# Optimization experiments

Hardware: AMD Instinct MI355X
Metric: run time of the kernel (lower is better)

The kernel has to match this reference:

```python
import jax, jax.numpy as jnp
import numpy as np

ALPHA = 0.2  # LeakyReLU negative slope


def setup_inputs() -> dict:
    key = jax.random.key(0)
    k1, k2, k3, k4 = jax.random.split(key, 4)
    B, N, F_IN, F_OUT = 4, 4096, 256, 256
    h = jax.random.normal(k1, (B, N, F_IN), dtype=jnp.float32)
    adj = jax.random.randint(k2, (B, N, N), 0, 2, dtype=jnp.int32)
    # xavier_normal with gain=1.414: std = gain*sqrt(2/(fan_in+fan_out))
    std_W = 1.414 * np.sqrt(2.0 / (F_IN + F_OUT))
    W = jax.random.normal(k3, (F_IN, F_OUT), dtype=jnp.float32) * std_W
    std_a = 1.414 * np.sqrt(2.0 / (1 + 2 * F_OUT))
    a = jax.random.normal(k4, (1, 2 * F_OUT), dtype=jnp.float32) * std_a
    return {"h": h, "adj": adj, "W": W, "a": a}


def reference(h, adj, W, a):
    # h: [B, N, F_in], adj: [B, N, N] (0/1), W: [F_in, F_out], a: [1, 2*F_out]
    F_out = W.shape[1]
    Hh = jnp.einsum('bni,io->bno', h, W)               # [B, N, F_out]
    a_src = a[0, :F_out]                                # attends to edge source i
    a_dst = a[0, F_out:]                                # attends to edge target j
    s = jnp.einsum('bno,o->bn', Hh, a_src)              # [B, N]
    d = jnp.einsum('bno,o->bn', Hh, a_dst)              # [B, N]
    # score(i,j) = a . concat(Hh_i, Hh_j) = s_i + d_j
    logits = s[:, :, None] + d[:, None, :]              # [B, N, N]
    # edge_e = exp(-leakyrelu(score)) only on edges (adj nonzero), else 0
    e = jnp.where(adj != 0,
                  jnp.exp(-jax.nn.leaky_relu(logits, negative_slope=ALPHA)),
                  jnp.zeros((), dtype=Hh.dtype))        # [B, N, N]
    rowsum = jnp.sum(e, axis=-1, keepdims=True)         # [B, N, 1]
    # rows with zero sum keep divisor 1 (as in the torch code)
    rowsum = jnp.where(rowsum == 0.0, 1.0, rowsum)
    h_prime = jnp.einsum('bnm,bmo->bno', e, Hh) / rowsum  # [B, N, F_out]
    return jax.nn.elu(h_prime)  # concat=True branch
```

## Files before the change

kernel.cpp:

```cpp
#include <hip/hip_runtime.h>

#define LRELU_ALPHA 0.2f

typedef __bf16 bf16x8 __attribute__((ext_vector_type(8)));
typedef unsigned short u16;
typedef unsigned short u16x4 __attribute__((ext_vector_type(4)));
typedef unsigned short u16x8 __attribute__((ext_vector_type(8)));
typedef unsigned int   u32x2 __attribute__((ext_vector_type(2)));
typedef float f32x4 __attribute__((ext_vector_type(4)));
typedef int int4v __attribute__((ext_vector_type(4)));

__device__ __forceinline__ u16 f2bf(float f) {
  unsigned int u = __float_as_uint(f);
  u += 0x7fffu + ((u >> 16) & 1u);
  return (u16)(u >> 16);
}

__global__ __launch_bounds__(256) void wcast(const float* __restrict__ W,
                                             u16* __restrict__ WbT) {
  int idx = blockIdx.x * 256 + threadIdx.x;
  WbT[idx] = f2bf(W[(idx & 255) * 256 + (idx >> 8)]);
}

__global__ __launch_bounds__(256) void gemm1(const float* __restrict__ h,
                                             const u16* __restrict__ WbT,
                                             const float* __restrict__ a,
                                             u16* __restrict__ HhT,
                                             float* __restrict__ sbuf,
                                             float* __restrict__ dbuf) {
  const int tid = threadIdx.x, bid = blockIdx.x;
  const int l = tid & 63, w = tid >> 6;
  const int lr = l & 15;
  const int lk = (l >> 4) << 3;
  const int rowA = bid * 64 + 16 * w + lr;
  const float* hrow = h + (size_t)rowA * 256 + lk;

  f32x4 acc[16];
#pragma unroll
  for (int n = 0; n < 16; ++n) acc[n] = (f32x4){0.f, 0.f, 0.f, 0.f};

  for (int k0 = 0; k0 < 256; k0 += 32) {
    f32x4 a0 = *(const f32x4*)(hrow + k0);
    f32x4 a1 = *(const f32x4*)(hrow + k0 + 4);
    u16x8 au;
    au[0] = f2bf(a0[0]); au[1] = f2bf(a0[1]); au[2] = f2bf(a0[2]); au[3] = f2bf(a0[3]);
    au[4] = f2bf(a1[0]); au[5] = f2bf(a1[1]); au[6] = f2bf(a1[2]); au[7] = f2bf(a1[3]);
    bf16x8 af = __builtin_bit_cast(bf16x8, au);
#pragma unroll
    for (int n = 0; n < 16; ++n) {
      int4v bv = *(const int4v*)(WbT + (size_t)(16 * n + lr) * 256 + k0 + lk);
      bf16x8 bf = __builtin_bit_cast(bf16x8, bv);
      acc[n] = __builtin_amdgcn_mfma_f32_16x16x32_bf16(af, bf, acc[n], 0, 0, 0);
    }
  }

  float sp[4] = {0.f, 0.f, 0.f, 0.f}, dp[4] = {0.f, 0.f, 0.f, 0.f};
#pragma unroll
  for (int n = 0; n < 16; ++n) {
    int col = 16 * n + lr;
    float as = a[col];
    float ad = a[256 + col];
#pragma unroll
    for (int rr = 0; rr < 4; ++rr) {
      int row = bid * 64 + 16 * w + ((l >> 4) << 2) + rr;
      int bb = row >> 12, nl = row & 4095;
      float v = acc[n][rr];
      HhT[((size_t)(bb * 256 + col)) * 4096 + nl] = f2bf(v);
      sp[rr] += v * as;
      dp[rr] += v * ad;
    }
  }
#pragma unroll
  for (int rr = 0; rr < 4; ++rr) {
#pragma unroll
    for (int off = 1; off < 16; off <<= 1) {
      sp[rr] += __shfl_xor(sp[rr], off);
      dp[rr] += __shfl_xor(dp[rr], off);
    }
  }
  if ((l & 15) == 0) {
#pragma unroll
    for (int rr = 0; rr < 4; ++rr) {
      int row = bid * 64 + 16 * w + ((l >> 4) << 2) + rr;
      sbuf[row] = sp[rr];
      dbuf[row] = dp[rr];
    }
  }
}

__global__ __launch_bounds__(256, 2) void gat_main(const int* __restrict__ adj,
                                                   const u16* __restrict__ HhT,
                                                   const float* __restrict__ s,
                                                   const float* __restrict__ d,
                                                   float* __restrict__ out) {
  __shared__ __align__(16) u16 At[2][32 * 40];
  __shared__ __align__(16) u16 Bt[2][256 * 40];
  __shared__ float d_lds[4096];
  __shared__ float rs_lds[32];

  const int tid = threadIdx.x;
  const int bid = blockIdx.x;
  const int xcd = bid & 7;
  const int b = xcd >> 1;
  const int tile = (bid >> 3) | ((xcd & 1) << 6);
  const int rowbase = tile << 5;

  for (int i = tid; i < 4096; i += 256) d_lds[i] = d[b * 4096 + i];

  const int r = tid >> 3, q = tid & 7;
  const float s_row = s[b * 4096 + rowbase + r];

  const int4v* aptr = (const int4v*)(adj + ((size_t)(b * 4096 + rowbase + r)) * 4096);
  const int cr = tid >> 2, cp = tid & 3;
  const int4v* bp0 = (const int4v*)HhT + (((size_t)(b * 256 + cr      )) << 9) + cp;
  const int4v* bp1 = (const int4v*)HhT + (((size_t)(b * 256 + cr +  64)) << 9) + cp;
  const int4v* bp2 = (const int4v*)HhT + (((size_t)(b * 256 + cr + 128)) << 9) + cp;
  const int4v* bp3 = (const int4v*)HhT + (((size_t)(b * 256 + cr + 192)) << 9) + cp;

  const int l = tid & 63, w = tid >> 6;
  const int lr = l & 15, lk = (l >> 4) << 3;
  const int row0 = 16 * (w & 1);
  const int colb = 128 * (w >> 1);

  f32x4 acc[8];
#pragma unroll
  for (int n = 0; n < 8; ++n) acc[n] = (f32x4){0.f, 0.f, 0.f, 0.f};
  float rowacc = 0.f;

  __syncthreads();

  int4v pa_a = aptr[q],        pa_b = aptr[8 + q];
  int4v pb0_a = bp0[0], pb1_a = bp1[0], pb2_a = bp2[0], pb3_a = bp3[0];
  int4v pb0_b = bp0[4], pb1_b = bp1[4], pb2_b = bp2[4], pb3_b = bp3[4];

#define SUBSTEP(BUF, PA, PB0, PB1, PB2, PB3, CURSTEP, NEXTSTEP)               \
  {                                                                           \
    const int k0_ = (CURSTEP) << 5;                                           \
    f32x4 dv = *(const f32x4*)&d_lds[k0_ + q * 4];                            \
    int aj[4] = {PA.x, PA.y, PA.z, PA.w};                                     \
    u16x4 ep;                                                                 \
    _Pragma("unroll")                                                         \
    for (int j = 0; j < 4; ++j) {                                             \
      float lg = s_row + dv[j];                                               \
      float t = lg > 0.f ? lg : LRELU_ALPHA * lg;                             \
      float e = (aj[j] != 0) ? __expf(-t) : 0.f;                              \
      rowacc += e;                                                            \
      ep[j] = f2bf(e);                                                        \
    }                                                                         \
    *(u32x2*)&At[BUF][r * 40 + q * 4] = __builtin_bit_cast(u32x2, ep);        \
    *(int4v*)&Bt[BUF][(cr      ) * 40 + cp * 8] = PB0;                        \
    *(int4v*)&Bt[BUF][(cr +  64) * 40 + cp * 8] = PB1;                        \
    *(int4v*)&Bt[BUF][(cr + 128) * 40 + cp * 8] = PB2;                        \
    *(int4v*)&Bt[BUF][(cr + 192) * 40 + cp * 8] = PB3;                        \
    {                                                                         \
      const int ns_ = (NEXTSTEP);                                             \
      PA  = aptr[ns_ * 8 + q];                                                \
      PB0 = bp0[ns_ << 2];                                                    \
      PB1 = bp1[ns_ << 2];                                                    \
      PB2 = bp2[ns_ << 2];                                                    \
      PB3 = bp3[ns_ << 2];                                                    \
    }                                                                         \
    asm volatile("s_waitcnt lgkmcnt(0)" ::: "memory");                        \
    __builtin_amdgcn_s_barrier();                                             \
    {                                                                         \
      bf16x8 af = __builtin_bit_cast(bf16x8,                                  \
          *(const int4v*)&At[BUF][(row0 + lr) * 40 + lk]);                    \
      _Pragma("unroll")                                                       \
      for (int n = 0; n < 8; ++n) {                                           \
        bf16x8 bf = __builtin_bit_cast(bf16x8,                                \
            *(const int4v*)&Bt[BUF][(colb + 16 * n + lr) * 40 + lk]);         \
        acc[n] = __builtin_amdgcn_mfma_f32_16x16x32_bf16(af, bf, acc[n],      \
                                                         0, 0, 0);            \
      }                                                                       \
    }                                                                         \
  }

  for (int sp2 = 0; sp2 < 128; sp2 += 2) {
    int na = sp2 + 2; if (na > 127) na = 127;
    int nb = sp2 + 3; if (nb > 127) nb = 127;
    SUBSTEP(0, pa_a, pb0_a, pb1_a, pb2_a, pb3_a, sp2, na)
    SUBSTEP(1, pa_b, pb0_b, pb1_b, pb2_b, pb3_b, sp2 + 1, nb)
  }
#undef SUBSTEP

  float rsum = rowacc;
  rsum += __shfl_xor(rsum, 1);
  rsum += __shfl_xor(rsum, 2);
  rsum += __shfl_xor(rsum, 4);
  if (q == 0) rs_lds[r] = (rsum == 0.f) ? 1.f : rsum;
  __syncthreads();

#pragma unroll
  for (int rr = 0; rr < 4; ++rr) {
    int rin = row0 + ((l >> 4) << 2) + rr;
    float inv = 1.f / rs_lds[rin];
    size_t obase = ((size_t)(b * 4096 + rowbase + rin)) * 256 + colb;
#pragma unroll
    for (int n = 0; n < 8; ++n) {
      float v = acc[n][rr] * inv;
      out[obase + 16 * n + lr] = v > 0.f ? v : (__expf(v) - 1.f);
    }
  }
}

extern "C" void kernel_launch(void* const* d_in, const int* in_sizes, int n_in,
                              void* d_out, int out_size, void* d_ws, size_t ws_size,
                              hipStream_t stream) {
  const float* h = (const float*)d_in[0];
  const int* adj = (const int*)d_in[1];
  const float* W = (const float*)d_in[2];
  const float* a = (const float*)d_in[3];
  float* out = (float*)d_out;

  u16* WbT  = (u16*)d_ws;
  u16* HhT  = (u16*)((char*)d_ws + 131072);
  float* sb = (float*)((char*)d_ws + 131072 + 8388608);
  float* db = sb + 16384;

  hipLaunchKernelGGL(wcast,    dim3(256), dim3(256), 0, stream, W, WbT);
  hipLaunchKernelGGL(gemm1,    dim3(256), dim3(256), 0, stream, h, WbT, a, HhT, sb, db);
  hipLaunchKernelGGL(gat_main, dim3(512), dim3(256), 0, stream, adj, HhT, sb, db, out);
}
```

Measured before the change: 176.9 us.

## Compute attention weights directly in MFMA A-fragment registers and deepen prefetch

Each lane now computes the exp(-leakyrelu) edge weights for exactly the A-fragment elements it feeds to the MFMA, so the A tile no longer round-trips through LDS and the d vector is read from global memory instead of staged in shared memory. Adjacency, d and HhT loads are prefetched four steps ahead instead of two, and setprio plus sched_barrier are added around the MFMA block. The cost is that each weight is computed redundantly by the two wave columns (waves 0/2 and 1/3 share rows), and register pressure grows with more prefetch buffers, which could hurt occupancy at the 256x2 launch bound.

```diff
diff --git a/kernel.cpp b/kernel.cpp
--- a/kernel.cpp
+++ b/kernel.cpp
@@ -4,9 +4,7 @@
 
 typedef __bf16 bf16x8 __attribute__((ext_vector_type(8)));
 typedef unsigned short u16;
-typedef unsigned short u16x4 __attribute__((ext_vector_type(4)));
 typedef unsigned short u16x8 __attribute__((ext_vector_type(8)));
-typedef unsigned int   u32x2 __attribute__((ext_vector_type(2)));
 typedef float f32x4 __attribute__((ext_vector_type(4)));
 typedef int int4v __attribute__((ext_vector_type(4)));
 
@@ -93,9 +91,7 @@
                                                    const float* __restrict__ s,
                                                    const float* __restrict__ d,
                                                    float* __restrict__ out) {
-  __shared__ __align__(16) u16 At[2][32 * 40];
   __shared__ __align__(16) u16 Bt[2][256 * 40];
-  __shared__ float d_lds[4096];
   __shared__ float rs_lds[32];
 
   const int tid = threadIdx.x;
@@ -105,66 +101,73 @@
   const int tile = (bid >> 3) | ((xcd & 1) << 6);
   const int rowbase = tile << 5;
 
-  for (int i = tid; i < 4096; i += 256) d_lds[i] = d[b * 4096 + i];
-
-  const int r = tid >> 3, q = tid & 7;
-  const float s_row = s[b * 4096 + rowbase + r];
-
-  const int4v* aptr = (const int4v*)(adj + ((size_t)(b * 4096 + rowbase + r)) * 4096);
+  const int l = tid & 63, w = tid >> 6;
+  const int lr = l & 15, lkg = l >> 4, lk = lkg << 3;
+  const int row0 = 16 * (w & 1);
+  const int colb = 128 * (w >> 1);
+
+  const int myrow = rowbase + row0 + lr;
+  const float s_row = s[b * 4096 + myrow];
+
+  const int4v* aptr = (const int4v*)(adj + ((size_t)(b * 4096 + myrow)) * 4096 + lk);
+  const f32x4* dptr = (const f32x4*)(d + b * 4096 + lk);
+
   const int cr = tid >> 2, cp = tid & 3;
   const int4v* bp0 = (const int4v*)HhT + (((size_t)(b * 256 + cr      )) << 9) + cp;
   const int4v* bp1 = (const int4v*)HhT + (((size_t)(b * 256 + cr +  64)) << 9) + cp;
   const int4v* bp2 = (const int4v*)HhT + (((size_t)(b * 256 + cr + 128)) << 9) + cp;
   const int4v* bp3 = (const int4v*)HhT + (((size_t)(b * 256 + cr + 192)) << 9) + cp;
 
-  const int l = tid & 63, w = tid >> 6;
-  const int lr = l & 15, lk = (l >> 4) << 3;
-  const int row0 = 16 * (w & 1);
-  const int colb = 128 * (w >> 1);
-
   f32x4 acc[8];
 #pragma unroll
   for (int n = 0; n < 8; ++n) acc[n] = (f32x4){0.f, 0.f, 0.f, 0.f};
-  float rowacc = 0.f;
-
-  __syncthreads();
-
-  int4v pa_a = aptr[q],        pa_b = aptr[8 + q];
-  int4v pb0_a = bp0[0], pb1_a = bp1[0], pb2_a = bp2[0], pb3_a = bp3[0];
-  int4v pb0_b = bp0[4], pb1_b = bp1[4], pb2_b = bp2[4], pb3_b = bp3[4];
-
-#define SUBSTEP(BUF, PA, PB0, PB1, PB2, PB3, CURSTEP, NEXTSTEP)               \
+  float racc = 0.f;
+
+  int4v S0a0, S0a1, S1a0, S1a1, S2a0, S2a1, S3a0, S3a1;
+  f32x4 S0d0, S0d1, S1d0, S1d1, S2d0, S2d1, S3d0, S3d1;
+  int4v S0b0, S0b1, S0b2, S0b3, S1b0, S1b1, S1b2, S1b3;
+  int4v S2b0, S2b1, S2b2, S2b3, S3b0, S3b1, S3b2, S3b3;
+
+#define PREF_B(S, STEP) { const int i_ = (STEP) << 2;                         \
+    S##b0 = bp0[i_]; S##b1 = bp1[i_]; S##b2 = bp2[i_]; S##b3 = bp3[i_]; }
+#define PREF_AD(S, STEP) { const int i_ = (STEP) << 3;                        \
+    S##a0 = aptr[i_]; S##a1 = aptr[i_ + 1];                                   \
+    S##d0 = dptr[i_]; S##d1 = dptr[i_ + 1]; }
+
+  PREF_B(S0, 0) PREF_AD(S0, 0)
+  PREF_B(S1, 1) PREF_AD(S1, 1)
+  PREF_B(S2, 2) PREF_AD(S2, 2)
+  PREF_B(S3, 3) PREF_AD(S3, 3)
+
+#define SUBSTEP(BUF, S, NXT)                                                  \
   {                                                                           \
-    const int k0_ = (CURSTEP) << 5;                                           \
-    f32x4 dv = *(const f32x4*)&d_lds[k0_ + q * 4];                            \
-    int aj[4] = {PA.x, PA.y, PA.z, PA.w};                                     \
-    u16x4 ep;                                                                 \
-    _Pragma("unroll")                                                         \
-    for (int j = 0; j < 4; ++j) {                                             \
-      float lg = s_row + dv[j];                                               \
-      float t = lg > 0.f ? lg : LRELU_ALPHA * lg;                             \
-      float e = (aj[j] != 0) ? __expf(-t) : 0.f;                              \
-      rowacc += e;                                                            \
-      ep[j] = f2bf(e);                                                        \
+    *(int4v*)&Bt[BUF][(cr      ) * 40 + cp * 8] = S##b0;                      \
+    *(int4v*)&Bt[BUF][(cr +  64) * 40 + cp * 8] = S##b1;                      \
+    *(int4v*)&Bt[BUF][(cr + 128) * 40 + cp * 8] = S##b2;                      \
+    *(int4v*)&Bt[BUF][(cr + 192) * 40 + cp * 8] = S##b3;                      \
+    PREF_B(S, NXT)                                                            \
+    u16x8 au_;                                                                \
+    {                                                                         \
+      int aj[8] = {S##a0.x, S##a0.y, S##a0.z, S##a0.w,                        \
+                   S##a1.x, S##a1.y, S##a1.z, S##a1.w};                       \
+      float dv[8] = {S##d0[0], S##d0[1], S##d0[2], S##d0[3],                  \
+                     S##d1[0], S##d1[1], S##d1[2], S##d1[3]};                 \
+      _Pragma("unroll")                                                       \
+      for (int j = 0; j < 8; ++j) {                                           \
+        float lg = s_row + dv[j];                                             \
+        float t = fmaxf(lg, LRELU_ALPHA * lg);                                \
+        float e = (aj[j] != 0) ? __expf(-t) : 0.f;                            \
+        racc += e;                                                            \
+        au_[j] = f2bf(e);                                                     \
+      }                                                                       \
     }                                                                         \
-    *(u32x2*)&At[BUF][r * 40 + q * 4] = __builtin_bit_cast(u32x2, ep);        \
-    *(int4v*)&Bt[BUF][(cr      ) * 40 + cp * 8] = PB0;                        \
-    *(int4v*)&Bt[BUF][(cr +  64) * 40 + cp * 8] = PB1;                        \
-    *(int4v*)&Bt[BUF][(cr + 128) * 40 + cp * 8] = PB2;                        \
-    *(int4v*)&Bt[BUF][(cr + 192) * 40 + cp * 8] = PB3;                        \
-    {                                                                         \
-      const int ns_ = (NEXTSTEP);                                             \
-      PA  = aptr[ns_ * 8 + q];                                                \
-      PB0 = bp0[ns_ << 2];                                                    \
-      PB1 = bp1[ns_ << 2];                                                    \
-      PB2 = bp2[ns_ << 2];                                                    \
-      PB3 = bp3[ns_ << 2];                                                    \
-    }                                                                         \
+    PREF_AD(S, NXT)                                                           \
     asm volatile("s_waitcnt lgkmcnt(0)" ::: "memory");                        \
     __builtin_amdgcn_s_barrier();                                             \
+    __builtin_amdgcn_sched_barrier(0);                                        \
     {                                                                         \
-      bf16x8 af = __builtin_bit_cast(bf16x8,                                  \
-          *(const int4v*)&At[BUF][(row0 + lr) * 40 + lk]);                    \
+      bf16x8 af = __builtin_bit_cast(bf16x8, au_);                            \
+      __builtin_amdgcn_s_setprio(1);                                          \
       _Pragma("unroll")                                                       \
       for (int n = 0; n < 8; ++n) {                                           \
         bf16x8 bf = __builtin_bit_cast(bf16x8,                                \
@@ -172,27 +175,33 @@
         acc[n] = __builtin_amdgcn_mfma_f32_16x16x32_bf16(af, bf, acc[n],      \
                                                          0, 0, 0);            \
       }                                                                       \
+      __builtin_amdgcn_s_setprio(0);                                          \
     }                                                                         \
   }
 
-  for (int sp2 = 0; sp2 < 128; sp2 += 2) {
-    int na = sp2 + 2; if (na > 127) na = 127;
-    int nb = sp2 + 3; if (nb > 127) nb = 127;
-    SUBSTEP(0, pa_a, pb0_a, pb1_a, pb2_a, pb3_a, sp2, na)
-    SUBSTEP(1, pa_b, pb0_b, pb1_b, pb2_b, pb3_b, sp2 + 1, nb)
+  for (int k = 0; k < 128; k += 4) {
+    int n0 = k + 4, n1 = k + 5, n2 = k + 6, n3 = k + 7;
+    if (n0 > 127) n0 = 127;
+    if (n1 > 127) n1 = 127;
+    if (n2 > 127) n2 = 127;
+    if (n3 > 127) n3 = 127;
+    SUBSTEP(0, S0, n0)
+    SUBSTEP(1, S1, n1)
+    SUBSTEP(0, S2, n2)
+    SUBSTEP(1, S3, n3)
   }
 #undef SUBSTEP
-
-  float rsum = rowacc;
-  rsum += __shfl_xor(rsum, 1);
-  rsum += __shfl_xor(rsum, 2);
-  rsum += __shfl_xor(rsum, 4);
-  if (q == 0) rs_lds[r] = (rsum == 0.f) ? 1.f : rsum;
+#undef PREF_B
+#undef PREF_AD
+
+  racc += __shfl_xor(racc, 16);
+  racc += __shfl_xor(racc, 32);
+  if (w < 2 && lkg == 0) rs_lds[row0 + lr] = (racc == 0.f) ? 1.f : racc;
   __syncthreads();
 
 #pragma unroll
   for (int rr = 0; rr < 4; ++rr) {
-    int rin = row0 + ((l >> 4) << 2) + rr;
+    int rin = row0 + (lkg << 2) + rr;
     float inv = 1.f / rs_lds[rin];
     size_t obase = ((size_t)(b * 4096 + rowbase + rin)) * 256 + colb;
 #pragma unroll
```

New measurement: 222.9 us. 26.0% more time.
